# Kernel tuning notes

Measured on AMD Instinct MI355X. Metric: run time of the kernel, lower is better.

The kernel has to match this reference:

```python
import jax, jax.numpy as jnp
import numpy as np

N_NODES = 100000
N_EDGES = 800000
N_REL = 16
D = 64
EPS = 1e-12
NEG_SLOPE = 0.01  # nn.LeakyReLU default


def _l2norm(x):
    # matches torch F.normalize(p=2, dim=-1)
    n = jnp.sqrt(jnp.sum(x * x, axis=-1, keepdims=True))
    return x / jnp.maximum(n, EPS)


def setup_inputs() -> dict:
    key = jax.random.key(0)
    ks = jax.random.split(key, 12)
    inp = {
        "src": jax.random.randint(ks[0], (N_EDGES,), 0, N_NODES, dtype=jnp.int32),
        "dst": jax.random.randint(ks[1], (N_EDGES,), 0, N_NODES, dtype=jnp.int32),
        "etype": jax.random.randint(ks[2], (N_EDGES,), 0, N_REL, dtype=jnp.int32),
        "ent_embed": jax.random.normal(ks[3], (N_NODES, D), jnp.float32) * 0.1,
        "ent_transfer": jax.random.normal(ks[4], (N_NODES, D), jnp.float32) * 0.1,
        "rel_embed": jax.random.normal(ks[5], (N_REL, D), jnp.float32) * 0.1,
        "rel_transfer": jax.random.normal(ks[6], (N_REL, D), jnp.float32) * 0.1,
        "W1_0": jax.random.normal(ks[7], (64, 32), jnp.float32) * (1.0 / np.sqrt(64)),
        "b1_0": jnp.zeros((32,), jnp.float32),
        "W2_0": jax.random.normal(ks[8], (64, 32), jnp.float32) * (1.0 / np.sqrt(64)),
        "b2_0": jnp.zeros((32,), jnp.float32),
        "W1_1": jax.random.normal(ks[9], (32, 16), jnp.float32) * (1.0 / np.sqrt(32)),
        "b1_1": jnp.zeros((16,), jnp.float32),
        "W2_1": jax.random.normal(ks[10], (32, 16), jnp.float32) * (1.0 / np.sqrt(32)),
        "b2_1": jnp.zeros((16,), jnp.float32),
    }
    return inp


def _compute_att(src, dst, etype, ent_embed, ent_transfer, rel_embed, rel_transfer):
    # per-edge gathers: h = dst node, t = src node (KGAT att_score convention)
    h_e = ent_embed[dst]          # [E, D]
    t_e = ent_embed[src]          # [E, D]
    h_p = ent_transfer[dst]
    t_p = ent_transfer[src]
    r_p = rel_transfer[etype]     # [E, D]
    r_e = rel_embed[etype]        # [E, D]
    # TransD projection + L2 normalize
    Mrt = _l2norm(t_e + jnp.sum(t_e * t_p, -1, keepdims=True) * r_p)
    Mrh = _l2norm(h_e + jnp.sum(h_e * h_p, -1, keepdims=True) * r_p)
    att = jnp.sum(Mrt * jnp.tanh(Mrh + r_e), axis=-1)  # [E]
    # edge softmax grouped by destination node
    m = jax.ops.segment_max(att, dst, num_segments=N_NODES)
    m = jnp.where(jnp.isfinite(m), m, 0.0)
    ex = jnp.exp(att - m[dst])
    s = jax.ops.segment_sum(ex, dst, num_segments=N_NODES)
    return ex / jnp.maximum(s[dst], EPS)  # [E]


def _bi_layer(node, N_h, W1, b1, W2, b2):
    out1 = jax.nn.leaky_relu((node + N_h) @ W1 + b1, NEG_SLOPE)
    out2 = jax.nn.leaky_relu((node * N_h) @ W2 + b2, NEG_SLOPE)
    return out1 + out2


def reference(src, dst, etype, ent_embed, ent_transfer, rel_embed, rel_transfer,
              W1_0, b1_0, W2_0, b2_0, W1_1, b1_1, W2_1, b2_1):
    att = _compute_att(src, dst, etype, ent_embed, ent_transfer, rel_embed, rel_transfer)
    node = ent_embed
    all_embed = [node]
    for (W1, b1, W2, b2) in [(W1_0, b1_0, W2_0, b2_0), (W1_1, b1_1, W2_1, b2_1)]:
        # u_mul_e + sum: N_h[v] = sum_{e: dst(e)=v} att_e * node[src(e)]
        msg = att[:, None] * node[src]                      # [E, d]
        N_h = jax.ops.segment_sum(msg, dst, num_segments=N_NODES)
        node = _bi_layer(node, N_h, W1, b1, W2, b2)         # dropout p=0 (eval)
        all_embed.append(_l2norm(node))
    return jnp.concatenate(all_embed, axis=1)  # [N, 64+32+16]
```

## Files before the change

### kernel.cpp

```cpp
#include <hip/hip_runtime.h>
#include <math.h>

#define EPSF 1e-12f
#define LOG2E 1.44269504f

template <int CTRL>
__device__ __forceinline__ float dppadd(float x) {
    union { float f; int i; } u, r;
    u.f = x;
    r.i = __builtin_amdgcn_update_dpp(0, u.i, CTRL, 0xF, 0xF, false);
    return x + r.f;
}
__device__ __forceinline__ float red16(float v) {
    v = dppadd<0xB1>(v); v = dppadd<0x4E>(v);
    v = dppadd<0x141>(v); v = dppadd<0x140>(v);
    return v;
}
__device__ __forceinline__ float red8(float v) {
    v = dppadd<0xB1>(v); v = dppadd<0x4E>(v); v = dppadd<0x141>(v);
    return v;
}
__device__ __forceinline__ float xor8add(float v) {
    return dppadd<0x128>(v);
}

__device__ __forceinline__ float fast_tanh(float x) {
    float E = __builtin_amdgcn_exp2f(x * (2.0f * LOG2E));
    return 1.0f - 2.0f * __builtin_amdgcn_rcpf(E + 1.0f);
}

__device__ __forceinline__ float inv_norm(float x) {
    return __builtin_amdgcn_rsqf(fmaxf(x, 1e-24f));
}

__device__ __forceinline__ float leaky(float x) {
    return x > 0.0f ? x : 0.01f * x;
}

__global__ __launch_bounds__(256) void prep(
    const float* __restrict__ ent, const float* __restrict__ entT,
    float* __restrict__ dot, const int* __restrict__ dst,
    int* __restrict__ deg, int N16, int E) {
    int gid = blockIdx.x * 256 + threadIdx.x;
    if (gid < N16) {
        int v = gid >> 4, lane = gid & 15;
        const float4 a = *(const float4*)(ent  + (size_t)v * 64 + lane * 4);
        const float4 b = *(const float4*)(entT + (size_t)v * 64 + lane * 4);
        float d = red16(a.x*b.x + a.y*b.y + a.z*b.z + a.w*b.w);
        if (lane == 0) dot[v] = d;
    } else {
        int e = gid - N16;
        if (e < E) atomicAdd(&deg[dst[e]], 1);
    }
}


__global__ __launch_bounds__(256) void scan_reduce(
    const int* __restrict__ deg, int* __restrict__ part, int N) {
    __shared__ int sh[256];
    int t = threadIdx.x, i = blockIdx.x * 256 + t;
    sh[t] = (i < N) ? deg[i] : 0;
    __syncthreads();
    for (int off = 128; off > 0; off >>= 1) {
        if (t < off) sh[t] += sh[t + off];
        __syncthreads();
    }
    if (t == 0) part[blockIdx.x] = sh[0];
}

__global__ __launch_bounds__(1024) void scan_part(int* __restrict__ part, int nb) {
    __shared__ int sh[1024];
    int t = threadIdx.x;
    int x = (t < nb) ? part[t] : 0;
    sh[t] = x;
    __syncthreads();
    for (int off = 1; off < 1024; off <<= 1) {
        int y = (t >= off) ? sh[t - off] : 0;
        __syncthreads();
        sh[t] += y;
        __syncthreads();
    }
    if (t < nb) part[t] = sh[t] - x;
}

__global__ __launch_bounds__(256) void scan_write(
    int* __restrict__ rowptr, const int* __restrict__ part, int N) {
    __shared__ int sh[256];
    int t = threadIdx.x, i = blockIdx.x * 256 + t;
    int x = (i < N) ? rowptr[i] : 0;
    sh[t] = x;
    __syncthreads();
    for (int off = 1; off < 256; off <<= 1) {
        int y = (t >= off) ? sh[t - off] : 0;
        __syncthreads();
        sh[t] += y;
        __syncthreads();
    }
    if (i < N) rowptr[i] = part[blockIdx.x] + sh[t] - x;
}

__global__ __launch_bounds__(256) void scatter_edges(
    const int* __restrict__ src, const int* __restrict__ dst,
    const int* __restrict__ ety, const float* __restrict__ dot,
    int* __restrict__ rowptr, int2* __restrict__ spk2, int E) {
    int e = blockIdx.x * 256 + threadIdx.x;
    if (e < E) {
        int sv = src[e];
        int slot = atomicAdd(&rowptr[dst[e]], 1);
        spk2[slot] = make_int2(sv | (ety[e] << 20), __float_as_int(dot[sv]));
    }
}

__global__ __launch_bounds__(256) void fused_l0(
    const int* __restrict__ rowptr, const int2* __restrict__ spk2,
    const float* __restrict__ ent, const float* __restrict__ dot,
    const float* __restrict__ relE, const float* __restrict__ relT,
    const float* __restrict__ W1, const float* __restrict__ b1,
    const float* __restrict__ W2, const float* __restrict__ b2,
    float* __restrict__ exatt, float* __restrict__ sinv,
    float* __restrict__ node1raw, float* __restrict__ out, int N) {
    __shared__ float  al[8][64];
    __shared__ float  bl[8][64];
    __shared__ float  rT[16][64];
    __shared__ float  rE[16][64];
    __shared__ float4 WtA[16 * 32];
    __shared__ float4 WtB[16 * 32];
    int t = threadIdx.x;

    {
        int r = t >> 4, c = (t & 15) * 4;
        *(float4*)&rT[r][c] = *(const float4*)(relT + r * 64 + c);
        *(float4*)&rE[r][c] = *(const float4*)(relE + r * 64 + c);
        int j = t & 31;
        for (int dd = t >> 5; dd < 16; dd += 8) {
            int d4 = dd * 4;
            WtA[dd * 32 + j] = make_float4(W1[(d4+0)*32 + j], W1[(d4+1)*32 + j],
                                           W1[(d4+2)*32 + j], W1[(d4+3)*32 + j]);
            WtB[dd * 32 + j] = make_float4(W2[(d4+0)*32 + j], W2[(d4+1)*32 + j],
                                           W2[(d4+2)*32 + j], W2[(d4+3)*32 + j]);
        }
    }
    __syncthreads();

    int nv = t >> 5, half = (t >> 4) & 1, lane = t & 15;
    int v = blockIdx.x * 8 + nv;
    if (v >= N) return;

    int s = v ? rowptr[v - 1] : 0;
    int epos = rowptr[v];
    int deg = epos - s;
    int mid = s + ((deg + 1) >> 1);
    int hs   = half ? mid  : s;
    int hend = half ? epos : mid;

    const float4 he = *(const float4*)(ent + (size_t)v * 64 + lane * 4);
    float dh = dot[v];

    float4 macc = {0.f, 0.f, 0.f, 0.f};
    float sumex = 0.0f;

    for (int base = hs; base < hend; base += 16) {
        int rem = hend - base;
        int cnt = rem < 16 ? rem : 16;
        int2 ms = spk2[base + (lane < rem ? lane : rem - 1)];
        float myex = 0.0f;

        int pk0 = __shfl(ms.x, 0, 16);
        int pk1 = __shfl(ms.x, cnt > 1 ? 1 : 0, 16);
        float sd0 = __int_as_float(__shfl(ms.y, 0, 16));
        float sd1 = __int_as_float(__shfl(ms.y, cnt > 1 ? 1 : 0, 16));
        float4 te0 = *(const float4*)(ent + (size_t)(pk0 & 0xFFFFF) * 64 + lane * 4);
        float4 te1 = *(const float4*)(ent + (size_t)(pk1 & 0xFFFFF) * 64 + lane * 4);

        for (int k = 0; k < cnt; k += 2) {
            float4 ta = te0, tb = te1;
            float  sa = sd0, sb = sd1;
            int rva = (pk0 >> 20) & 15;
            int rvb = (pk1 >> 20) & 15;
            bool hasb = (k + 1) < cnt;

            if (k + 2 < cnt) {
                int i2 = k + 2, i3 = (k + 3 < cnt) ? (k + 3) : (k + 2);
                pk0 = __shfl(ms.x, i2, 16);
                pk1 = __shfl(ms.x, i3, 16);
                sd0 = __int_as_float(__shfl(ms.y, i2, 16));
                sd1 = __int_as_float(__shfl(ms.y, i3, 16));
                te0 = *(const float4*)(ent + (size_t)(pk0 & 0xFFFFF) * 64 + lane * 4);
                te1 = *(const float4*)(ent + (size_t)(pk1 & 0xFFFFF) * 64 + lane * 4);
            }

            const float4 rpa = *(const float4*)&rT[rva][lane * 4];
            const float4 rea = *(const float4*)&rE[rva][lane * 4];
            const float4 rpb = *(const float4*)&rT[rvb][lane * 4];
            const float4 reb = *(const float4*)&rE[rvb][lane * 4];

            float4 mta, mha, mtb, mhb;
            mta.x = ta.x + sa * rpa.x; mta.y = ta.y + sa * rpa.y;
            mta.z = ta.z + sa * rpa.z; mta.w = ta.w + sa * rpa.w;
            mha.x = he.x + dh * rpa.x; mha.y = he.y + dh * rpa.y;
            mha.z = he.z + dh * rpa.z; mha.w = he.w + dh * rpa.w;
            mtb.x = tb.x + sb * rpb.x; mtb.y = tb.y + sb * rpb.y;
            mtb.z = tb.z + sb * rpb.z; mtb.w = tb.w + sb * rpb.w;
            mhb.x = he.x + dh * rpb.x; mhb.y = he.y + dh * rpb.y;
            mhb.z = he.z + dh * rpb.z; mhb.w = he.w + dh * rpb.w;

            float ssta = red16(mta.x*mta.x + mta.y*mta.y + mta.z*mta.z + mta.w*mta.w);
            float ssha = red16(mha.x*mha.x + mha.y*mha.y + mha.z*mha.z + mha.w*mha.w);
            float sstb = red16(mtb.x*mtb.x + mtb.y*mtb.y + mtb.z*mtb.z + mtb.w*mtb.w);
            float sshb = red16(mhb.x*mhb.x + mhb.y*mhb.y + mhb.z*mhb.z + mhb.w*mhb.w);
            float ita = inv_norm(ssta), iha = inv_norm(ssha);
            float itb = inv_norm(sstb), ihb = inv_norm(sshb);

            float txa = fast_tanh(mha.x * iha + rea.x);
            float tya = fast_tanh(mha.y * iha + rea.y);
            float tza = fast_tanh(mha.z * iha + rea.z);
            float twa = fast_tanh(mha.w * iha + rea.w);
            float txb = fast_tanh(mhb.x * ihb + reb.x);
            float tyb = fast_tanh(mhb.y * ihb + reb.y);
            float tzb = fast_tanh(mhb.z * ihb + reb.z);
            float twb = fast_tanh(mhb.w * ihb + reb.w);

            float atta = ita * red16(mta.x*txa + mta.y*tya + mta.z*tza + mta.w*twa);
            float attb = itb * red16(mtb.x*txb + mtb.y*tyb + mtb.z*tzb + mtb.w*twb);

            float exa  = __builtin_amdgcn_exp2f(atta * LOG2E);
            float exbR = __builtin_amdgcn_exp2f(attb * LOG2E);
            float exb  = hasb ? exbR : 0.0f;

            myex = (lane == k) ? exa : myex;
            myex = (lane == k + 1) ? exbR : myex;

            sumex += exa + exb;
            macc.x += exa * ta.x + exb * tb.x;
            macc.y += exa * ta.y + exb * tb.y;
            macc.z += exa * ta.z + exb * tb.z;
            macc.w += exa * ta.w + exb * tb.w;
        }
        if (lane < cnt) exatt[base + lane] = myex;
    }

    sumex  += __shfl_xor(sumex,  16, 32);
    macc.x += __shfl_xor(macc.x, 16, 32);
    macc.y += __shfl_xor(macc.y, 16, 32);
    macc.z += __shfl_xor(macc.z, 16, 32);
    macc.w += __shfl_xor(macc.w, 16, 32);

    float inv = 1.0f / fmaxf(sumex, EPSF);
    if ((t & 31) == 0) sinv[v] = inv;
    macc.x *= inv; macc.y *= inv; macc.z *= inv; macc.w *= inv;

    if (!half) {
        *(float4*)(out + (size_t)v * 112 + lane * 4) = he;
        float4 av, bv;
        av.x = he.x + macc.x; av.y = he.y + macc.y;
        av.z = he.z + macc.z; av.w = he.w + macc.w;
        bv.x = he.x * macc.x; bv.y = he.y * macc.y;
        bv.z = he.z * macc.z; bv.w = he.w * macc.w;
        *(float4*)&al[nv][lane * 4] = av;
        *(float4*)&bl[nv][lane * 4] = bv;
    }

    int j = t & 31;
    float acc1 = b1[j], acc2 = b2[j];
    #pragma unroll
    for (int dd = 0; dd < 16; ++dd) {
        float4 a4 = *(const float4*)&al[nv][dd * 4];
        float4 b4 = *(const float4*)&bl[nv][dd * 4];
        float4 wa = WtA[dd * 32 + j];
        float4 wb = WtB[dd * 32 + j];
        acc1 += a4.x*wa.x + a4.y*wa.y + a4.z*wa.z + a4.w*wa.w;
        acc2 += b4.x*wb.x + b4.y*wb.y + b4.z*wb.z + b4.w*wb.w;
    }
    node1raw[(size_t)v * 32 + j] = leaky(acc1) + leaky(acc2);
}

__global__ __launch_bounds__(256) void fused_l1(
    const int* __restrict__ rowptr, const int2* __restrict__ spk2,
    const float* __restrict__ exatt, const float* __restrict__ sinv,
    const float* __restrict__ node1raw,
    const float* __restrict__ W1, const float* __restrict__ b1,
    const float* __restrict__ W2, const float* __restrict__ b2,
    float* __restrict__ out, int N) {
    __shared__ float  A[16][32];
    __shared__ float  B[16][32];
    __shared__ float4 WtC[8 * 16];
    __shared__ float4 WtD[8 * 16];
    int t = threadIdx.x;

    {
        int tt = t & 127;
        int j = tt & 15, dd = tt >> 4;
        int d4 = dd * 4;
        const float* W = (t < 128) ? W1 : W2;
        float4* Wt = (t < 128) ? WtC : WtD;
        Wt[dd * 16 + j] = make_float4(W[(d4+0)*16 + j], W[(d4+1)*16 + j],
                                      W[(d4+2)*16 + j], W[(d4+3)*16 + j]);
    }
    __syncthreads();

    int nv = t >> 4, half = (t >> 3) & 1, lane = t & 7;
    int v = blockIdx.x * 16 + nv;
    if (v >= N) return;

    int s = v ? rowptr[v - 1] : 0;
    int epos = rowptr[v];
    int deg = epos - s;
    int mid = s + ((deg + 1) >> 1);
    int hs   = half ? mid  : s;
    int hend = half ? epos : mid;

    float4 n = *(const float4*)(node1raw + (size_t)v * 32 + lane * 4);
    float4 acc = {0.f, 0.f, 0.f, 0.f};

    for (int base = hs; base < hend; base += 8) {
        int rem = hend - base;
        int cnt = rem < 8 ? rem : 8;
        int idx = base + (lane < rem ? lane : rem - 1);
        int   mypk = spk2[idx].x;
        float myex = exatt[idx];

        int pk0 = __shfl(mypk, 0, 8);
        int pk1 = __shfl(mypk, cnt > 1 ? 1 : 0, 8);
        float4 x0 = *(const float4*)(node1raw + (size_t)(pk0 & 0xFFFFF) * 32 + lane * 4);
        float4 x1 = *(const float4*)(node1raw + (size_t)(pk1 & 0xFFFFF) * 32 + lane * 4);

        for (int k = 0; k < cnt; k += 2) {
            float4 xa = x0, xb = x1;
            float aa = __shfl(myex, k, 8);
            float ab = __shfl(myex, (k + 1 < cnt) ? (k + 1) : k, 8);
            if (!((k + 1) < cnt)) ab = 0.0f;

            if (k + 2 < cnt) {
                pk0 = __shfl(mypk, k + 2, 8);
                pk1 = __shfl(mypk, (k + 3 < cnt) ? (k + 3) : (k + 2), 8);
                x0 = *(const float4*)(node1raw + (size_t)(pk0 & 0xFFFFF) * 32 + lane * 4);
                x1 = *(const float4*)(node1raw + (size_t)(pk1 & 0xFFFFF) * 32 + lane * 4);
            }
            acc.x += aa * xa.x + ab * xb.x;
            acc.y += aa * xa.y + ab * xb.y;
            acc.z += aa * xa.z + ab * xb.z;
            acc.w += aa * xa.w + ab * xb.w;
        }
    }
    acc.x = xor8add(acc.x);
    acc.y = xor8add(acc.y);
    acc.z = xor8add(acc.z);
    acc.w = xor8add(acc.w);

    float inv = sinv[v];
    acc.x *= inv; acc.y *= inv; acc.z *= inv; acc.w *= inv;

    float ss = red8(n.x*n.x + n.y*n.y + n.z*n.z + n.w*n.w);
    float inv1 = inv_norm(ss);

    if (!half) {
        float4 nn = {n.x*inv1, n.y*inv1, n.z*inv1, n.w*inv1};
        *(float4*)(out + (size_t)v * 112 + 64 + lane * 4) = nn;
        float4 av = {n.x + acc.x, n.y + acc.y, n.z + acc.z, n.w + acc.w};
        float4 bv = {n.x * acc.x, n.y * acc.y, n.z * acc.z, n.w * acc.w};
        *(float4*)&A[nv][lane * 4] = av;
        *(float4*)&B[nv][lane * 4] = bv;
    }

    int j = t & 15;
    float a1 = b1[j], a2 = b2[j];
    #pragma unroll
    for (int dd = 0; dd < 8; ++dd) {
        float4 a4 = *(const float4*)&A[nv][dd * 4];
        float4 b4 = *(const float4*)&B[nv][dd * 4];
        float4 wc = WtC[dd * 16 + j];
        float4 wd = WtD[dd * 16 + j];
        a1 += a4.x*wc.x + a4.y*wc.y + a4.z*wc.z + a4.w*wc.w;
        a2 += b4.x*wd.x + b4.y*wd.y + b4.z*wd.z + b4.w*wd.w;
    }
    float tot = leaky(a1) + leaky(a2);
    float s2 = red16(tot * tot);
    float inv2 = inv_norm(s2);
    out[(size_t)v * 112 + 96 + j] = tot * inv2;
}

extern "C" void kernel_launch(void* const* d_in, const int* in_sizes, int n_in,
                              void* d_out, int out_size, void* d_ws, size_t ws_size,
                              hipStream_t stream) {
    const int*   src  = (const int*)d_in[0];
    const int*   dst  = (const int*)d_in[1];
    const int*   ety  = (const int*)d_in[2];
    const float* ent  = (const float*)d_in[3];
    const float* entT = (const float*)d_in[4];
    const float* relE = (const float*)d_in[5];
    const float* relT = (const float*)d_in[6];
    const float* W1_0 = (const float*)d_in[7];
    const float* b1_0 = (const float*)d_in[8];
    const float* W2_0 = (const float*)d_in[9];
    const float* b2_0 = (const float*)d_in[10];
    const float* W1_1 = (const float*)d_in[11];
    const float* b1_1 = (const float*)d_in[12];
    const float* W2_1 = (const float*)d_in[13];
    const float* b2_1 = (const float*)d_in[14];
    float* out = (float*)d_out;

    const int E = in_sizes[0];
    const int N = in_sizes[3] / 64;
    const int nb = (N + 255) / 256;

    auto al256 = [](size_t x) { return (x + 255) & ~(size_t)255; };
    char* ws = (char*)d_ws;
    size_t offExatt = 0;
    size_t offS     = al256(offExatt + (size_t)E * 4);
    size_t offDot   = al256(offS + (size_t)N * 4);
    size_t offRow   = al256(offDot + (size_t)N * 4);
    size_t offSpk   = al256(offRow + (size_t)N * 4);
    size_t offPart  = al256(offSpk + (size_t)E * 8);
    size_t offN1    = al256(offPart + (size_t)nb * 4);
    float* exatt    = (float*)(ws + offExatt);
    float* sinv     = (float*)(ws + offS);
    float* dot      = (float*)(ws + offDot);
    int*   rowptr   = (int*)(ws + offRow);
    int2*  spk2     = (int2*)(ws + offSpk);
    int*   part     = (int*)(ws + offPart);
    float* node1raw = (float*)(ws + offN1);

    hipMemsetAsync(rowptr, 0, (size_t)N * 4, stream);
    int N16 = N * 16;
    prep<<<(N16 + E + 255) / 256, 256, 0, stream>>>(ent, entT, dot, dst,
                                                    rowptr, N16, E);
    scan_reduce<<<nb, 256, 0, stream>>>(rowptr, part, N);
    scan_part<<<1, 1024, 0, stream>>>(part, nb);
    scan_write<<<nb, 256, 0, stream>>>(rowptr, part, N);
    int blkE = (E + 255) / 256;
    scatter_edges<<<blkE, 256, 0, stream>>>(src, dst, ety, dot, rowptr, spk2, E);

    fused_l0<<<(N + 7) / 8, 256, 0, stream>>>(
        rowptr, spk2, ent, dot, relE, relT,
        W1_0, b1_0, W2_0, b2_0, exatt, sinv, node1raw, out, N);

    fused_l1<<<(N + 15) / 16, 256, 0, stream>>>(
        rowptr, spk2, exatt, sinv, node1raw,
        W1_1, b1_1, W2_1, b2_1, out, N);
}
```

Baseline: 210.3 us.

## Widen per-node edge parallelism to four lane groups in both fused layers

Each destination node now gets a full 64-lane wavefront in layer 0 (and 32 lanes in layer 1), split into four 16- or 8-lane groups that each handle one edge per iteration. Before, two halves each handled two edges. The dense bi-interaction matmul is split across the extra lanes: one half computes the W1 path and the other the W2 path, combined with a shuffle. The aim is more memory-level parallelism per node for the short average degree (about 8) and fewer serialized iterations. The cost is half as many nodes per block, so more blocks, extra cross-group shuffles, and idle lanes on low-degree nodes.

```diff
diff --git a/kernel.cpp b/kernel.cpp
--- a/kernel.cpp
+++ b/kernel.cpp
@@ -19,9 +19,6 @@
 __device__ __forceinline__ float red8(float v) {
     v = dppadd<0xB1>(v); v = dppadd<0x4E>(v); v = dppadd<0x141>(v);
     return v;
-}
-__device__ __forceinline__ float xor8add(float v) {
-    return dppadd<0x128>(v);
 }
 
 __device__ __forceinline__ float fast_tanh(float x) {
@@ -119,8 +116,8 @@
     const float* __restrict__ W2, const float* __restrict__ b2,
     float* __restrict__ exatt, float* __restrict__ sinv,
     float* __restrict__ node1raw, float* __restrict__ out, int N) {
-    __shared__ float  al[8][64];
-    __shared__ float  bl[8][64];
+    __shared__ float  al[4][64];
+    __shared__ float  bl[4][64];
     __shared__ float  rT[16][64];
     __shared__ float  rE[16][64];
     __shared__ float4 WtA[16 * 32];
@@ -142,16 +139,15 @@
     }
     __syncthreads();
 
-    int nv = t >> 5, half = (t >> 4) & 1, lane = t & 15;
-    int v = blockIdx.x * 8 + nv;
+    int wv = t >> 6;
+    int l64 = t & 63;
+    int grp = (t >> 4) & 3;
+    int lane = t & 15;
+    int v = blockIdx.x * 4 + wv;
     if (v >= N) return;
 
     int s = v ? rowptr[v - 1] : 0;
     int epos = rowptr[v];
-    int deg = epos - s;
-    int mid = s + ((deg + 1) >> 1);
-    int hs   = half ? mid  : s;
-    int hend = half ? epos : mid;
 
     const float4 he = *(const float4*)(ent + (size_t)v * 64 + lane * 4);
     float dh = dot[v];
@@ -159,119 +155,95 @@
     float4 macc = {0.f, 0.f, 0.f, 0.f};
     float sumex = 0.0f;
 
-    for (int base = hs; base < hend; base += 16) {
-        int rem = hend - base;
-        int cnt = rem < 16 ? rem : 16;
-        int2 ms = spk2[base + (lane < rem ? lane : rem - 1)];
-        float myex = 0.0f;
-
-        int pk0 = __shfl(ms.x, 0, 16);
-        int pk1 = __shfl(ms.x, cnt > 1 ? 1 : 0, 16);
-        float sd0 = __int_as_float(__shfl(ms.y, 0, 16));
-        float sd1 = __int_as_float(__shfl(ms.y, cnt > 1 ? 1 : 0, 16));
-        float4 te0 = *(const float4*)(ent + (size_t)(pk0 & 0xFFFFF) * 64 + lane * 4);
-        float4 te1 = *(const float4*)(ent + (size_t)(pk1 & 0xFFFFF) * 64 + lane * 4);
-
-        for (int k = 0; k < cnt; k += 2) {
-            float4 ta = te0, tb = te1;
-            float  sa = sd0, sb = sd1;
-            int rva = (pk0 >> 20) & 15;
-            int rvb = (pk1 >> 20) & 15;
-            bool hasb = (k + 1) < cnt;
-
-            if (k + 2 < cnt) {
-                int i2 = k + 2, i3 = (k + 3 < cnt) ? (k + 3) : (k + 2);
-                pk0 = __shfl(ms.x, i2, 16);
-                pk1 = __shfl(ms.x, i3, 16);
-                sd0 = __int_as_float(__shfl(ms.y, i2, 16));
-                sd1 = __int_as_float(__shfl(ms.y, i3, 16));
-                te0 = *(const float4*)(ent + (size_t)(pk0 & 0xFFFFF) * 64 + lane * 4);
-                te1 = *(const float4*)(ent + (size_t)(pk1 & 0xFFFFF) * 64 + lane * 4);
+    for (int cb = s; cb < epos; cb += 64) {
+        int cnt = epos - cb; if (cnt > 64) cnt = 64;
+        int2 ms = spk2[cb + (l64 < cnt ? l64 : cnt - 1)];
+        int iters = (cnt + 3) >> 2;
+
+        int cur = grp < cnt ? grp : cnt - 1;
+        int pk = __shfl(ms.x, cur, 64);
+        float sd = __int_as_float(__shfl(ms.y, cur, 64));
+        float4 te = *(const float4*)(ent + (size_t)(pk & 0xFFFFF) * 64 + lane * 4);
+
+        for (int i = 0; i < iters; ++i) {
+            float4 ta = te;
+            float  sa = sd;
+            int pkc = pk;
+            bool valid = (i * 4 + grp) < cnt;
+            int sidx = cb + i * 4 + grp;
+
+            if (i + 1 < iters) {
+                int nxt = (i + 1) * 4 + grp; if (nxt >= cnt) nxt = cnt - 1;
+                pk = __shfl(ms.x, nxt, 64);
+                sd = __int_as_float(__shfl(ms.y, nxt, 64));
+                te = *(const float4*)(ent + (size_t)(pk & 0xFFFFF) * 64 + lane * 4);
             }
 
-            const float4 rpa = *(const float4*)&rT[rva][lane * 4];
-            const float4 rea = *(const float4*)&rE[rva][lane * 4];
-            const float4 rpb = *(const float4*)&rT[rvb][lane * 4];
-            const float4 reb = *(const float4*)&rE[rvb][lane * 4];
-
-            float4 mta, mha, mtb, mhb;
-            mta.x = ta.x + sa * rpa.x; mta.y = ta.y + sa * rpa.y;
-            mta.z = ta.z + sa * rpa.z; mta.w = ta.w + sa * rpa.w;
-            mha.x = he.x + dh * rpa.x; mha.y = he.y + dh * rpa.y;
-            mha.z = he.z + dh * rpa.z; mha.w = he.w + dh * rpa.w;
-            mtb.x = tb.x + sb * rpb.x; mtb.y = tb.y + sb * rpb.y;
-            mtb.z = tb.z + sb * rpb.z; mtb.w = tb.w + sb * rpb.w;
-            mhb.x = he.x + dh * rpb.x; mhb.y = he.y + dh * rpb.y;
-            mhb.z = he.z + dh * rpb.z; mhb.w = he.w + dh * rpb.w;
-
-            float ssta = red16(mta.x*mta.x + mta.y*mta.y + mta.z*mta.z + mta.w*mta.w);
-            float ssha = red16(mha.x*mha.x + mha.y*mha.y + mha.z*mha.z + mha.w*mha.w);
-            float sstb = red16(mtb.x*mtb.x + mtb.y*mtb.y + mtb.z*mtb.z + mtb.w*mtb.w);
-            float sshb = red16(mhb.x*mhb.x + mhb.y*mhb.y + mhb.z*mhb.z + mhb.w*mhb.w);
-            float ita = inv_norm(ssta), iha = inv_norm(ssha);
-            float itb = inv_norm(sstb), ihb = inv_norm(sshb);
-
-            float txa = fast_tanh(mha.x * iha + rea.x);
-            float tya = fast_tanh(mha.y * iha + rea.y);
-            float tza = fast_tanh(mha.z * iha + rea.z);
-            float twa = fast_tanh(mha.w * iha + rea.w);
-            float txb = fast_tanh(mhb.x * ihb + reb.x);
-            float tyb = fast_tanh(mhb.y * ihb + reb.y);
-            float tzb = fast_tanh(mhb.z * ihb + reb.z);
-            float twb = fast_tanh(mhb.w * ihb + reb.w);
-
-            float atta = ita * red16(mta.x*txa + mta.y*tya + mta.z*tza + mta.w*twa);
-            float attb = itb * red16(mtb.x*txb + mtb.y*tyb + mtb.z*tzb + mtb.w*twb);
-
-            float exa  = __builtin_amdgcn_exp2f(atta * LOG2E);
-            float exbR = __builtin_amdgcn_exp2f(attb * LOG2E);
-            float exb  = hasb ? exbR : 0.0f;
-
-            myex = (lane == k) ? exa : myex;
-            myex = (lane == k + 1) ? exbR : myex;
-
-            sumex += exa + exb;
-            macc.x += exa * ta.x + exb * tb.x;
-            macc.y += exa * ta.y + exb * tb.y;
-            macc.z += exa * ta.z + exb * tb.z;
-            macc.w += exa * ta.w + exb * tb.w;
+            int rv = (pkc >> 20) & 15;
+            const float4 rp = *(const float4*)&rT[rv][lane * 4];
+            const float4 re = *(const float4*)&rE[rv][lane * 4];
+
+            float4 mt, mh;
+            mt.x = ta.x + sa * rp.x; mt.y = ta.y + sa * rp.y;
+            mt.z = ta.z + sa * rp.z; mt.w = ta.w + sa * rp.w;
+            mh.x = he.x + dh * rp.x; mh.y = he.y + dh * rp.y;
+            mh.z = he.z + dh * rp.z; mh.w = he.w + dh * rp.w;
+
+            float sst = red16(mt.x*mt.x + mt.y*mt.y + mt.z*mt.z + mt.w*mt.w);
+            float ssh = red16(mh.x*mh.x + mh.y*mh.y + mh.z*mh.z + mh.w*mh.w);
+            float it = inv_norm(sst), ih = inv_norm(ssh);
+
+            float tx = fast_tanh(mh.x * ih + re.x);
+            float ty = fast_tanh(mh.y * ih + re.y);
+            float tz = fast_tanh(mh.z * ih + re.z);
+            float tw = fast_tanh(mh.w * ih + re.w);
+
+            float att = it * red16(mt.x*tx + mt.y*ty + mt.z*tz + mt.w*tw);
+            float exR = __builtin_amdgcn_exp2f(att * LOG2E);
+            float ex  = valid ? exR : 0.0f;
+            if (lane == 0 && valid) exatt[sidx] = exR;
+
+            sumex += ex;
+            macc.x += ex * ta.x; macc.y += ex * ta.y;
+            macc.z += ex * ta.z; macc.w += ex * ta.w;
         }
-        if (lane < cnt) exatt[base + lane] = myex;
-    }
-
-    sumex  += __shfl_xor(sumex,  16, 32);
-    macc.x += __shfl_xor(macc.x, 16, 32);
-    macc.y += __shfl_xor(macc.y, 16, 32);
-    macc.z += __shfl_xor(macc.z, 16, 32);
-    macc.w += __shfl_xor(macc.w, 16, 32);
+    }
+
+    sumex  += __shfl_xor(sumex,  16, 64); sumex  += __shfl_xor(sumex,  32, 64);
+    macc.x += __shfl_xor(macc.x, 16, 64); macc.x += __shfl_xor(macc.x, 32, 64);
+    macc.y += __shfl_xor(macc.y, 16, 64); macc.y += __shfl_xor(macc.y, 32, 64);
+    macc.z += __shfl_xor(macc.z, 16, 64); macc.z += __shfl_xor(macc.z, 32, 64);
+    macc.w += __shfl_xor(macc.w, 16, 64); macc.w += __shfl_xor(macc.w, 32, 64);
 
     float inv = 1.0f / fmaxf(sumex, EPSF);
-    if ((t & 31) == 0) sinv[v] = inv;
+    if (l64 == 0) sinv[v] = inv;
     macc.x *= inv; macc.y *= inv; macc.z *= inv; macc.w *= inv;
 
-    if (!half) {
+    if (l64 < 16) {
         *(float4*)(out + (size_t)v * 112 + lane * 4) = he;
         float4 av, bv;
         av.x = he.x + macc.x; av.y = he.y + macc.y;
         av.z = he.z + macc.z; av.w = he.w + macc.w;
         bv.x = he.x * macc.x; bv.y = he.y * macc.y;
         bv.z = he.z * macc.z; bv.w = he.w * macc.w;
-        *(float4*)&al[nv][lane * 4] = av;
-        *(float4*)&bl[nv][lane * 4] = bv;
-    }
-
-    int j = t & 31;
-    float acc1 = b1[j], acc2 = b2[j];
+        *(float4*)&al[wv][lane * 4] = av;
+        *(float4*)&bl[wv][lane * 4] = bv;
+    }
+
+    int j = l64 & 31;
+    bool second = l64 >= 32;
+    const float*  sv_ = second ? bl[wv] : al[wv];
+    const float4* Wt  = second ? WtB : WtA;
+    float acc = second ? b2[j] : b1[j];
     #pragma unroll
     for (int dd = 0; dd < 16; ++dd) {
-        float4 a4 = *(const float4*)&al[nv][dd * 4];
-        float4 b4 = *(const float4*)&bl[nv][dd * 4];
-        float4 wa = WtA[dd * 32 + j];
-        float4 wb = WtB[dd * 32 + j];
-        acc1 += a4.x*wa.x + a4.y*wa.y + a4.z*wa.z + a4.w*wa.w;
-        acc2 += b4.x*wb.x + b4.y*wb.y + b4.z*wb.z + b4.w*wb.w;
-    }
-    node1raw[(size_t)v * 32 + j] = leaky(acc1) + leaky(acc2);
+        float4 a4 = *(const float4*)&sv_[dd * 4];
+        float4 w  = Wt[dd * 32 + j];
+        acc += a4.x*w.x + a4.y*w.y + a4.z*w.z + a4.w*w.w;
+    }
+    float res = leaky(acc);
+    res += __shfl_xor(res, 32, 64);
+    if (!second) node1raw[(size_t)v * 32 + j] = res;
 }
 
 __global__ __launch_bounds__(256) void fused_l1(
@@ -281,8 +253,8 @@
     const float* __restrict__ W1, const float* __restrict__ b1,
     const float* __restrict__ W2, const float* __restrict__ b2,
     float* __restrict__ out, int N) {
-    __shared__ float  A[16][32];
-    __shared__ float  B[16][32];
+    __shared__ float  A[8][32];
+    __shared__ float  B[8][32];
     __shared__ float4 WtC[8 * 16];
     __shared__ float4 WtD[8 * 16];
     int t = threadIdx.x;
@@ -298,54 +270,50 @@
     }
     __syncthreads();
 
-    int nv = t >> 4, half = (t >> 3) & 1, lane = t & 7;
-    int v = blockIdx.x * 16 + nv;
+    int hv  = t >> 5;
+    int l32 = t & 31;
+    int grp = (t >> 3) & 3;
+    int lane = t & 7;
+    int v = blockIdx.x * 8 + hv;
     if (v >= N) return;
 
     int s = v ? rowptr[v - 1] : 0;
     int epos = rowptr[v];
-    int deg = epos - s;
-    int mid = s + ((deg + 1) >> 1);
-    int hs   = half ? mid  : s;
-    int hend = half ? epos : mid;
 
     float4 n = *(const float4*)(node1raw + (size_t)v * 32 + lane * 4);
     float4 acc = {0.f, 0.f, 0.f, 0.f};
 
-    for (int base = hs; base < hend; base += 8) {
-        int rem = hend - base;
-        int cnt = rem < 8 ? rem : 8;
-        int idx = base + (lane < rem ? lane : rem - 1);
-        int   mypk = spk2[idx].x;
-        float myex = exatt[idx];
-
-        int pk0 = __shfl(mypk, 0, 8);
-        int pk1 = __shfl(mypk, cnt > 1 ? 1 : 0, 8);
-        float4 x0 = *(const float4*)(node1raw + (size_t)(pk0 & 0xFFFFF) * 32 + lane * 4);
-        float4 x1 = *(const float4*)(node1raw + (size_t)(pk1 & 0xFFFFF) * 32 + lane * 4);
-
-        for (int k = 0; k < cnt; k += 2) {
-            float4 xa = x0, xb = x1;
-            float aa = __shfl(myex, k, 8);
-            float ab = __shfl(myex, (k + 1 < cnt) ? (k + 1) : k, 8);
-            if (!((k + 1) < cnt)) ab = 0.0f;
-
-            if (k + 2 < cnt) {
-                pk0 = __shfl(mypk, k + 2, 8);
-                pk1 = __shfl(mypk, (k + 3 < cnt) ? (k + 3) : (k + 2), 8);
-                x0 = *(const float4*)(node1raw + (size_t)(pk0 & 0xFFFFF) * 32 + lane * 4);
-                x1 = *(const float4*)(node1raw + (size_t)(pk1 & 0xFFFFF) * 32 + lane * 4);
+    for (int cb = s; cb < epos; cb += 32) {
+        int cnt = epos - cb; if (cnt > 32) cnt = 32;
+        int ld = cb + (l32 < cnt ? l32 : cnt - 1);
+        int   mypk = spk2[ld].x;
+        float myex = exatt[ld];
+        int iters = (cnt + 3) >> 2;
+
+        int cur = grp < cnt ? grp : cnt - 1;
+        int pk = __shfl(mypk, cur, 32);
+        float a0 = __shfl(myex, cur, 32);
+        float4 x = *(const float4*)(node1raw + (size_t)(pk & 0xFFFFF) * 32 + lane * 4);
+
+        for (int i = 0; i < iters; ++i) {
+            float4 xa = x;
+            float aa = a0;
+            bool valid = (i * 4 + grp) < cnt;
+            if (i + 1 < iters) {
+                int nxt = (i + 1) * 4 + grp; if (nxt >= cnt) nxt = cnt - 1;
+                pk = __shfl(mypk, nxt, 32);
+                a0 = __shfl(myex, nxt, 32);
+                x = *(const float4*)(node1raw + (size_t)(pk & 0xFFFFF) * 32 + lane * 4);
             }
-            acc.x += aa * xa.x + ab * xb.x;
-            acc.y += aa * xa.y + ab * xb.y;
-            acc.z += aa * xa.z + ab * xb.z;
-            acc.w += aa * xa.w + ab * xb.w;
+            float w = valid ? aa : 0.0f;
+            acc.x += w * xa.x; acc.y += w * xa.y;
+            acc.z += w * xa.z; acc.w += w * xa.w;
         }
     }
-    acc.x = xor8add(acc.x);
-    acc.y = xor8add(acc.y);
-    acc.z = xor8add(acc.z);
-    acc.w = xor8add(acc.w);
+    acc.x += __shfl_xor(acc.x, 8, 32); acc.x += __shfl_xor(acc.x, 16, 32);
+    acc.y += __shfl_xor(acc.y, 8, 32); acc.y += __shfl_xor(acc.y, 16, 32);
+    acc.z += __shfl_xor(acc.z, 8, 32); acc.z += __shfl_xor(acc.z, 16, 32);
+    acc.w += __shfl_xor(acc.w, 8, 32); acc.w += __shfl_xor(acc.w, 16, 32);
 
     float inv = sinv[v];
     acc.x *= inv; acc.y *= inv; acc.z *= inv; acc.w *= inv;
@@ -353,30 +321,34 @@
     float ss = red8(n.x*n.x + n.y*n.y + n.z*n.z + n.w*n.w);
     float inv1 = inv_norm(ss);
 
-    if (!half) {
+    if (l32 < 8) {
         float4 nn = {n.x*inv1, n.y*inv1, n.z*inv1, n.w*inv1};
         *(float4*)(out + (size_t)v * 112 + 64 + lane * 4) = nn;
         float4 av = {n.x + acc.x, n.y + acc.y, n.z + acc.z, n.w + acc.w};
         float4 bv = {n.x * acc.x, n.y * acc.y, n.z * acc.z, n.w * acc.w};
-        *(float4*)&A[nv][lane * 4] = av;
-        *(float4*)&B[nv][lane * 4] = bv;
-    }
-
-    int j = t & 15;
-    float a1 = b1[j], a2 = b2[j];
+        *(float4*)&A[hv][lane * 4] = av;
+        *(float4*)&B[hv][lane * 4] = bv;
+    }
+
+    int j = l32 & 15;
+    bool second = l32 >= 16;
+    const float*  sv_ = second ? B[hv] : A[hv];
+    const float4* Wt  = second ? WtD : WtC;
+    float a1 = second ? b2[j] : b1[j];
     #pragma unroll
     for (int dd = 0; dd < 8; ++dd) {
-        float4 a4 = *(const float4*)&A[nv][dd * 4];
-        float4 b4 = *(const float4*)&B[nv][dd * 4];
-        float4 wc = WtC[dd * 16 + j];
-        float4 wd = WtD[dd * 16 + j];
-        a1 += a4.x*wc.x + a4.y*wc.y + a4.z*wc.z + a4.w*wc.w;
-        a2 += b4.x*wd.x + b4.y*wd.y + b4.z*wd.z + b4.w*wd.w;
-    }
-    float tot = leaky(a1) + leaky(a2);
-    float s2 = red16(tot * tot);
-    float inv2 = inv_norm(s2);
-    out[(size_t)v * 112 + 96 + j] = tot * inv2;
+        float4 a4 = *(const float4*)&sv_[dd * 4];
+        float4 w  = Wt[dd * 16 + j];
+        a1 += a4.x*w.x + a4.y*w.y + a4.z*w.z + a4.w*w.w;
+    }
+    float res = leaky(a1);
+    res += __shfl_xor(res, 16, 32);
+    if (!second) {
+        float tot = res;
+        float s2 = red16(tot * tot);
+        float inv2 = inv_norm(s2);
+        out[(size_t)v * 112 + 96 + j] = tot * inv2;
+    }
 }
 
 extern "C" void kernel_launch(void* const* d_in, const int* in_sizes, int n_in,
@@ -430,11 +402,11 @@
     int blkE = (E + 255) / 256;
     scatter_edges<<<blkE, 256, 0, stream>>>(src, dst, ety, dot, rowptr, spk2, E);
 
-    fused_l0<<<(N + 7) / 8, 256, 0, stream>>>(
+    fused_l0<<<(N + 3) / 4, 256, 0, stream>>>(
         rowptr, spk2, ent, dot, relE, relT,
         W1_0, b1_0, W2_0, b2_0, exatt, sinv, node1raw, out, N);
 
-    fused_l1<<<(N + 15) / 16, 256, 0, stream>>>(
+    fused_l1<<<(N + 7) / 8, 256, 0, stream>>>(
         rowptr, spk2, exatt, sinv, node1raw,
         W1_1, b1_1, W2_1, b2_1, out, N);
 }
```

Measured after the change: 247.6 us. 17.8% more time.
